# Kernel tuning notes

Hardware: AMD Instinct MI355X
Metric: run time of the kernel (lower is better)

## Reference

```python
import jax, jax.numpy as jnp
import numpy as np
from jax import lax

SCALES = [0.5, 1, 2]


def resize_bilinear_ac(x, oh, ow):
    """F.interpolate(mode='bilinear', align_corners=True) for NCHW x."""
    B, C, H, W = x.shape
    def coords(n_in, n_out):
        c = jnp.linspace(0.0, n_in - 1.0, n_out).astype(x.dtype)
        i0 = jnp.clip(jnp.floor(c).astype(jnp.int32), 0, n_in - 1)
        i1 = jnp.minimum(i0 + 1, n_in - 1)
        return i0, i1, c - i0.astype(x.dtype)
    y0, y1, wy = coords(H, oh)
    x0, x1, wx = coords(W, ow)
    top = x[:, :, y0, :] * (1 - wy)[:, None] + x[:, :, y1, :] * wy[:, None]
    return top[:, :, :, x0] * (1 - wx) + top[:, :, :, x1] * wx


def interpolate4d(t, oh, ow):
    """Geometry.interpolate4d: bilinear resize of both spatial pairs of [b,h1,w1,h2,w2]."""
    b, h1, w1, h2, w2 = t.shape
    t = t.reshape(b, h1, w1, h2 * w2).transpose(0, 3, 1, 2)
    t = resize_bilinear_ac(t, oh, ow)            # [b, h2*w2, oh, ow]
    t = t.reshape(b, h2, w2, oh * ow).transpose(0, 3, 1, 2)
    t = resize_bilinear_ac(t, oh, ow)            # [b, oh*ow, oh, ow]
    return t.reshape(b, oh, ow, oh, ow)


def conv2d_same(x, w):
    return lax.conv_general_dilated(x, w, (1, 1), [(1, 1), (1, 1)],
                                    dimension_numbers=('NCHW', 'OIHW', 'NCHW'))


def conv3d_same(x, w, p):
    return lax.conv_general_dilated(x, w, (1, 1, 1), [(p, p)] * 3,
                                    dimension_numbers=('NCDHW', 'OIDHW', 'NCDHW'))


def fast4d(corr, kernel, bias=None):
    """4D conv (stride 1, same zero-padding) via per-slice 3D convs, mirroring chm.fast4d.
    corr: [b, ci, sh, sw, th, tw]; kernel: [co, ci, k, k, k, k]."""
    b, ci, sh, sw, th, tw = corr.shape
    co, k = kernel.shape[0], kernel.shape[2]
    p = k // 2
    x = corr.transpose(0, 2, 1, 3, 4, 5).reshape(b * sh, ci, sw, th, tw)
    out = jnp.zeros((b, co, sh, sw, th, tw), corr.dtype)
    for pidx in range(k):
        ic = conv3d_same(x, kernel[:, :, pidx], p)
        ic = ic.reshape(b, sh, co, sw, th, tw).transpose(0, 2, 1, 3, 4, 5)
        a0, a1 = max(p - pidx, 0), min(sh, sh + p - pidx)
        s0, s1 = max(pidx - p, 0), min(sh, sh + pidx - p)
        out = out.at[:, :, a0:a1].add(ic[:, :, s0:s1])
    if bias is not None:
        out = out + bias.reshape(1, co, 1, 1, 1, 1)
    return out


def chm6d(corr, kernel):
    """6D conv with kernel (K,K,kk,kk,kk,kk), same zero-padding, no bias (chm.fast6d).
    corr: [b, 1, S, S, h, w, h, w]; kernel: [1, 1, K, K, kk, kk, kk, kk]."""
    b, _, S, _, h, w, _, _ = corr.shape
    K, kk = kernel.shape[2], kernel.shape[4]
    pk = K // 2
    x = corr.transpose(0, 2, 3, 1, 4, 5, 6, 7).reshape(b * S * S, 1, h, w, h, w)
    ker = kernel.reshape(1, K * K, kk, kk, kk, kk).swapaxes(0, 1)  # [K*K, 1, kk...]
    y = fast4d(x, ker).reshape(b, S, S, K * K, h, w, h, w)
    yp = jnp.pad(y, ((0, 0), (pk, pk), (pk, pk), (0, 0), (0, 0), (0, 0), (0, 0), (0, 0)))
    out = jnp.zeros((b, S, S, h, w, h, w), corr.dtype)
    for ki in range(K):
        for kj in range(K):
            out = out + yp[:, ki:ki + S, kj:kj + S, ki * K + kj]
    return out[:, None]


def mutual_nn_filter(cm):
    smax = jnp.max(cm, axis=2, keepdims=True)
    tmax = jnp.max(cm, axis=1, keepdims=True)
    smax = jnp.where(smax == 0, 1e-30, smax)
    tmax = jnp.where(tmax == 0, 1e-30, tmax)
    return cm * ((cm / smax) * (cm / tmax))


def build_correlation6d(src_feat, trg_feat, conv_ws):
    bsz, _, side, _ = src_feat.shape
    sfs, tfs = [], []
    for scale, w in zip(SCALES, conv_ws):
        s = int(np.floor(scale * side))
        sfs.append(conv2d_same(resize_bilinear_ac(src_feat, s, s), w))
        tfs.append(conv2d_same(resize_bilinear_ac(trg_feat, s, s), w))
    corr6d = []
    for sf in sfs:
        ch, ss = sf.shape[1], sf.shape[-1]
        sv = sf.reshape(bsz, ch, ss * ss).transpose(0, 2, 1)   # [b, ss^2, ch]
        sn = jnp.linalg.norm(sv, axis=2, keepdims=True)
        for tf in tfs:
            ts = tf.shape[-1]
            tv = tf.reshape(bsz, ch, ts * ts)                  # [b, ch, ts^2]
            tn = jnp.linalg.norm(tv, axis=1, keepdims=True)
            c = jnp.einsum('bsc,bct->bst', sv, tv) / (sn * tn)
            corr6d.append(interpolate4d(c.reshape(bsz, ss, ss, ts, ts), side, side))
    corr = jnp.stack(corr6d).reshape(3, 3, bsz, side, side, side, side)
    corr = corr.transpose(2, 0, 1, 3, 4, 5, 6)                 # [b, 3, 3, s, s, s, s]
    return jnp.maximum(corr, 0.0)


def chm_forward(src_feat, trg_feat, w0, w1, w2, k6, k4, b4):
    bsz, _, side, _ = src_feat.shape
    corr = build_correlation6d(src_feat, trg_feat, (w0, w1, w2))[:, None]
    corr = jax.nn.sigmoid(chm6d(corr, k6))                     # [b,1,3,3,h,w,h,w]
    h = w = side
    corr = corr.reshape(bsz, -1, h, w, h, w).max(axis=1)       # max over 9 scale pairs
    corr = interpolate4d(corr, 2 * h, 2 * w)[:, None]          # [b,1,2h,2w,2h,2w]
    corr = jax.nn.softplus(fast4d(corr, k4, b4)[:, 0])
    n = corr.shape[-1] ** 2
    return mutual_nn_filter(corr.reshape(bsz, n, n))


def setup_inputs() -> dict:
    key = jax.random.key(0)
    ks = jax.random.split(key, 8)
    b, fd, side = 4, 1024, 16
    w_std = 0.02  # ~kaiming for 3x3 conv with fan_in 1024*9
    return {
        'src_feat': jax.random.normal(ks[0], (b, fd, side, side), jnp.float32),
        'trg_feat': jax.random.normal(ks[1], (b, fd, side, side), jnp.float32),
        'conv_w0': jax.random.normal(ks[2], (fd // 4, fd, 3, 3), jnp.float32) * w_std,
        'conv_w1': jax.random.normal(ks[3], (fd // 4, fd, 3, 3), jnp.float32) * w_std,
        'conv_w2': jax.random.normal(ks[4], (fd // 4, fd, 3, 3), jnp.float32) * w_std,
        'chm6d_w': jax.random.normal(ks[5], (1, 1, 3, 3, 5, 5, 5, 5), jnp.float32) * 0.05,
        'chm4d_w': jax.random.normal(ks[6], (1, 1, 5, 5, 5, 5), jnp.float32) * 0.05,
        'chm4d_b': jnp.zeros((1,), jnp.float32),
    }


def reference(src_feat, trg_feat, conv_w0, conv_w1, conv_w2, chm6d_w, chm4d_w, chm4d_b):
    return chm_forward(src_feat, trg_feat, conv_w0, conv_w1, conv_w2, chm6d_w, chm4d_w, chm4d_b)
```

## Files before the change

### kernel.cpp

```cpp
#include <hip/hip_runtime.h>
#include <cstdint>
#include <cstddef>


#define DEVFN __device__ __forceinline__

typedef __attribute__((ext_vector_type(8))) short short8v;
typedef __attribute__((ext_vector_type(4))) float f32x4;
typedef unsigned int u32;

DEVFN void gl_lds16(const void* g, void* l){
  __builtin_amdgcn_global_load_lds(
      (const __attribute__((address_space(1))) u32*)g,
      (__attribute__((address_space(3))) u32*)l, 16, 0, 0);
}

constexpr size_t OFF_WB    = 0;
constexpr size_t OFF_P8    = 3538944;
constexpr size_t OFF_P16   = 3948544;
constexpr size_t OFF_P32   = 5275648;
constexpr size_t OFF_SF8   = 10010624;
constexpr size_t OFF_TF8   = 10076160;
constexpr size_t OFF_SF16  = 10141696;
constexpr size_t OFF_TF16  = 10403840;
constexpr size_t OFF_SF32  = 10665984;
constexpr size_t OFF_TF32  = 11714560;
constexpr size_t OFF_INVS  = 12763136;
constexpr size_t OFF_INVT  = 12768512;
constexpr size_t OFF_SMAX  = 12773888;
constexpr size_t OFF_TMAX  = 12777984;
constexpr size_t OFF_CORR6 = 12782080;
constexpr size_t OFF_CMAXP = OFF_CORR6 + 2359296 + 128;
constexpr size_t OFF_WA    = OFF_CMAXP + 131072;
constexpr size_t OFF_PARTK = OFF_WA + 96128;
constexpr size_t WS_FLOATS = OFF_PARTK + 2752512;

__device__ constexpr size_t PAIR_OFF[9] = {
  OFF_WB + 0,       OFF_WB + 16384,   OFF_WB + 81920,
  OFF_WB + 344064,  OFF_WB + 409600,  OFF_WB + 671744,
  OFF_WB + 1720320, OFF_WB + 1982464, OFF_WB + 3031040 };
constexpr size_t OFF_CL    = 0;
constexpr size_t OFF_MAXED = 9437184;
constexpr size_t OFF_INT32 = 262144;
constexpr size_t OFF_FB    = OFF_PARTK;

__device__ constexpr int SSARR[3] = {8, 16, 32};
__device__ constexpr int PAIR_START[9] = {0,4,20,84,100,164,420,484,740};

DEVFN unsigned short f2bf(float f){
  unsigned int u = __float_as_uint(f);
  return (unsigned short)((u + 0x7fffu + ((u >> 16) & 1u)) >> 16);
}
DEVFN float bf2f(unsigned short u){
  return __uint_as_float(((unsigned int)u) << 16);
}

__global__ __launch_bounds__(256) void k_wpack(const float* __restrict__ w0,
                                               const float* __restrict__ w1,
                                               const float* __restrict__ w2,
                                               float* __restrict__ wsf){
  int bx = blockIdx.x;
  int scale = bx >> 8, cg = (bx >> 4) & 15, ig = bx & 15;
  const float* w = (scale==0) ? w0 : (scale==1 ? w1 : w2);
  const int t = threadIdx.x;
  __shared__ float sW[16*580];
  const float* src = w + (size_t)cg*16*9216 + (size_t)ig*576;
  for (int i=t; i<9216; i+=256){
    int co = i/576, r = i%576;
    sW[co*580 + r] = src[(size_t)co*9216 + r];
  }
  __syncthreads();
  unsigned short* ob = (unsigned short*)(wsf + OFF_WB) + (size_t)scale*2359296;
  for (int f=t; f<1152; f+=256){
    int tap = f/128, rem = f%128, kcl = rem>>6, l = rem&63;
    int kc = ig*2 + kcl;
    int co = l & 15;
    int ciL = kcl*32 + ((l>>4)&3)*8;
    unsigned short* o = ob + ((size_t)tap*32768 + (size_t)kc*1024 + (size_t)cg*64 + l)*8;
    #pragma unroll
    for (int i=0;i<8;i++)
      o[i] = f2bf(sW[co*580 + (ciL+i)*9 + tap]);
  }
}

__global__ void k_wa(const float* __restrict__ k6, float* __restrict__ wsf){
  int gid = blockIdx.x*256 + threadIdx.x;
  if (gid >= 24000) return;
  int tap = gid / 192, rem = gid % 192;
  int kc = rem / 64, l = rem % 64;
  int d = tap % 5, ac = tap / 5, a = ac / 5, c = ac % 5;
  int so = l & 15, k8 = (l >> 4) * 8;
  unsigned short* o = (unsigned short*)(wsf + OFF_WA) + (size_t)gid*8;
  #pragma unroll
  for (int i=0;i<8;i++){
    int kg = kc*32 + k8 + i;
    int e = kg >> 4, pr = kg & 15;
    float v = 0.f;
    if (so < 9 && pr < 9 && e < 5){
      int pi = pr/3, pj = pr%3, sio = so/3, sjo = so%3;
      int ki = pi - sio + 1, kj = pj - sjo + 1;
      if (ki>=0 && ki<=2 && kj>=0 && kj<=2)
        v = k6[(((((ki*3+kj)*5 + a)*5 + c)*5 + d)*5) + e];
    }
    o[i] = f2bf(v);
  }
}

__global__ __launch_bounds__(256) void k_inpack(const float* __restrict__ src,
                                                const float* __restrict__ trg,
                                                float* __restrict__ wsf){
  int bt = blockIdx.x >> 6, cg = blockIdx.x & 63;
  int chbase = cg*16;
  int t = threadIdx.x;
  __shared__ float sIn[16][257];
  const float* gin = ((bt>=4)? trg : src) + ((size_t)(bt&3)*1024 + chbase)*256;
  #pragma unroll
  for (int i=0;i<16;i++){
    int idx = t + i*256; int ch = idx>>8, pos = idx&255;
    sIn[ch][pos] = gin[(size_t)ch*256 + pos];
  }
  __syncthreads();
  int ch = t & 15, pw = t >> 4;
  #pragma unroll 1
  for (int s=0; s<3; s++){
    int S = SSARR[s], Sp = S+2, Sp2 = Sp*Sp;
    size_t poff = (s==0)?OFF_P8 : (s==1)?OFF_P16 : OFF_P32;
    unsigned short* o = (unsigned short*)(wsf + poff) + (size_t)bt*Sp2*1024 + chbase + ch;
    float rs = 15.f/(float)(S-1);
    for (int i = pw; i < Sp2; i += 16){
      int py = i / Sp, px = i % Sp;
      float v = 0.f;
      if (py>0 && py<Sp-1 && px>0 && px<Sp-1){
        float cy = (float)(py-1)*rs, cx = (float)(px-1)*rs;
        int y0 = (int)cy; if (y0>15) y0=15; int y1 = (y0+1<16)?y0+1:15; float fy = cy-(float)y0;
        int x0 = (int)cx; if (x0>15) x0=15; int x1 = (x0+1<16)?x0+1:15; float fx = cx-(float)x0;
        v = (1.f-fy)*((1.f-fx)*sIn[ch][y0*16+x0] + fx*sIn[ch][y0*16+x1])
          +       fy*((1.f-fx)*sIn[ch][y1*16+x0] + fx*sIn[ch][y1*16+x1]);
      }
      o[(size_t)i*1024] = f2bf(v);
    }
  }
}

__global__ __launch_bounds__(256) void k_conv_mfma(float* __restrict__ wsf){
  int bs = (blockIdx.x & 7)*84 + (blockIdx.x >> 3);
  const int ks = bs & 1;
  int bx = bs >> 1;
  int scale, bt, cot, post, S, lgS;
  if (bx < 256)      { scale=2; S=32; lgS=5; bt=bx>>5; cot=(bx>>4)&1; post=bx&15; }
  else if (bx < 320) { int r=bx-256; scale=1; S=16; lgS=4; bt=r>>3; cot=(r>>2)&1; post=r&3; }
  else               { int r=bx-320; scale=0; S=8;  lgS=3; bt=r>>1; cot=r&1; post=0; }
  const int Sp = S+2, N = S*S;
  const unsigned short* WbS = (const unsigned short*)(wsf + OFF_WB) + (size_t)scale*2359296;
  size_t poff = scale==0?OFF_P8: scale==1?OFF_P16:OFF_P32;
  const unsigned short* Pb = (const unsigned short*)(wsf + poff) + (size_t)bt*Sp*Sp*1024;
  size_t obase = (scale==2) ? (bt>=4?OFF_TF32:OFF_SF32)
               : (scale==1) ? (bt>=4?OFF_TF16:OFF_SF16)
                            : (bt>=4?OFF_TF8 :OFF_SF8);
  if (ks) obase += OFF_PARTK - OFF_SF8;
  float* outp = wsf + obase + (size_t)(bt&3)*256*N;

  const int t = threadIdx.x, l = t&63, w = t>>6, wm = w&1, wn = w>>1;
  const int nc_base = cot*8;
  const int pos0 = post*64;
  const int it0 = ks*72, it1 = it0 + 72;

  __shared__ __align__(16) unsigned short Ab[2][8192];
  __shared__ __align__(16) unsigned short Bb[2][4096];

  f32x4 acc[4][2];
  #pragma unroll
  for (int i=0;i<4;i++)
    #pragma unroll
    for (int j=0;j<2;j++) acc[i][j] = (f32x4){0.f,0.f,0.f,0.f};

  auto STAGE = [&](int buf, int it){
    int tap = it>>4, kq = it&15;
    int dy = tap/3, dx = tap - dy*3;
    #pragma unroll
    for (int j=0;j<4;++j){
      int c = w + j*4;
      int kc = c>>3, nc = c&7;
      const unsigned short* src =
        WbS + ((((size_t)tap*32 + kq*2 + kc)*16 + nc_base + nc)*64 + l)*8;
      gl_lds16(src, &Ab[buf][c*512]);
    }
    #pragma unroll
    for (int j=0;j<2;++j){
      int c = w + j*4;
      int kc = c>>2, np = c&3;
      int pos = pos0 + np*16 + (l&15);
      int y = pos>>lgS, x = pos&(S-1);
      int row = (y+dy)*Sp + (x+dx);
      int ci = kq*64 + kc*32 + ((l>>4)<<3);
      gl_lds16(Pb + (size_t)row*1024 + ci, &Bb[buf][c*512]);
    }
  };

  STAGE(0, it0);
  __syncthreads();
  int buf = 0;
  #pragma unroll 1
  for (int it=it0; it<it1; ++it){
    if (it+1 < it1) STAGE(buf^1, it+1);
    #pragma unroll
    for (int kc=0; kc<2; ++kc){
      short8v a0 = *(const short8v*)&Ab[buf][((kc*8 + wm*4 + 0)*64 + l)*8];
      short8v a1 = *(const short8v*)&Ab[buf][((kc*8 + wm*4 + 1)*64 + l)*8];
      short8v a2 = *(const short8v*)&Ab[buf][((kc*8 + wm*4 + 2)*64 + l)*8];
      short8v a3 = *(const short8v*)&Ab[buf][((kc*8 + wm*4 + 3)*64 + l)*8];
      short8v b0 = *(const short8v*)&Bb[buf][((kc*4 + wn*2 + 0)*64 + l)*8];
      short8v b1 = *(const short8v*)&Bb[buf][((kc*4 + wn*2 + 1)*64 + l)*8];
      acc[0][0] = __builtin_amdgcn_mfma_f32_16x16x32_bf16(a0, b0, acc[0][0], 0,0,0);
      acc[1][0] = __builtin_amdgcn_mfma_f32_16x16x32_bf16(a1, b0, acc[1][0], 0,0,0);
      acc[2][0] = __builtin_amdgcn_mfma_f32_16x16x32_bf16(a2, b0, acc[2][0], 0,0,0);
      acc[3][0] = __builtin_amdgcn_mfma_f32_16x16x32_bf16(a3, b0, acc[3][0], 0,0,0);
      acc[0][1] = __builtin_amdgcn_mfma_f32_16x16x32_bf16(a0, b1, acc[0][1], 0,0,0);
      acc[1][1] = __builtin_amdgcn_mfma_f32_16x16x32_bf16(a1, b1, acc[1][1], 0,0,0);
      acc[2][1] = __builtin_amdgcn_mfma_f32_16x16x32_bf16(a2, b1, acc[2][1], 0,0,0);
      acc[3][1] = __builtin_amdgcn_mfma_f32_16x16x32_bf16(a3, b1, acc[3][1], 0,0,0);
    }
    __syncthreads();
    buf ^= 1;
  }

  const int r0 = (l>>4)*4, cl = l&15;
  float* ob = outp + (size_t)(cot*128 + wm*64)*N + pos0 + wn*32 + cl;
  #pragma unroll
  for (int mf=0; mf<4; ++mf)
    #pragma unroll
    for (int nf=0; nf<2; ++nf){
      float* op = ob + (size_t)(mf*16 + r0)*N + nf*16;
      #pragma unroll
      for (int i=0;i<4;++i) op[(size_t)i*N] = acc[mf][nf][i];
    }
}

__global__ void k_combine(float* __restrict__ ws){
  int i = blockIdx.x*256 + threadIdx.x;
  ws[OFF_SF8 + i] += ws[OFF_PARTK + i];
}

__global__ __launch_bounds__(256) void k_fbpack(float* __restrict__ ws){
  int bx = blockIdx.x;
  int tsr = bx/84, r = bx%84;
  int s, b, chunk;
  if (r < 4)       { s=0; b=r;        chunk=0; }
  else if (r < 20) { s=1; int q=r-4;  b=q>>2; chunk=q&3; }
  else             { s=2; int q=r-20; b=q>>4; chunk=q&15; }
  int P = SSARR[s]*SSARR[s];
  size_t fbase = (s==0)? (tsr?OFF_TF8 :OFF_SF8)
               : (s==1)? (tsr?OFF_TF16:OFF_SF16)
                       : (tsr?OFF_TF32:OFF_SF32);
  const float* src = ws + fbase + (size_t)b*256*P;
  int pos0 = chunk*64;
  const int t = threadIdx.x;
  __shared__ float tile[64][260];
  for (int i=0;i<64;i++){
    int idx = t + i*256; int ch = idx>>6, pl = idx&63;
    tile[pl][ch] = src[(size_t)ch*P + pos0 + pl];
  }
  __syncthreads();
  int rowbase = tsr*5376 + (s==0?0: s==1?256:1280) + b*P + pos0;
  unsigned short* FB = (unsigned short*)(ws + OFF_FB);
  for (int i=0;i<64;i++){
    int idx = t + i*256; int pl = idx>>8, ch = idx&255;
    FB[(size_t)(rowbase+pl)*256 + ch] = f2bf(tile[pl][ch]);
  }
}

__global__ void k_invnorm(float* __restrict__ ws){
  int gid = blockIdx.x*256 + threadIdx.x;
  int row = gid >> 4, sub = gid & 15;
  const unsigned short* fb = (const unsigned short*)(ws + OFF_FB)
                           + (size_t)row*256 + sub*16;
  float s = 0.f;
  #pragma unroll
  for (int i=0;i<2;i++){
    short8v v = *(const short8v*)(fb + i*8);
    #pragma unroll
    for (int j=0;j<8;j++){
      float f = bf2f(((unsigned short*)&v)[j]);
      s = fmaf(f, f, s);
    }
  }
  #pragma unroll
  for (int m=1; m<16; m<<=1) s += __shfl_xor(s, m);
  if (sub == 0){
    int tsr = row/5376, r = row%5376;
    ws[(tsr ? OFF_INVT : OFF_INVS) + r] = 1.f/sqrtf(s);
  }
}

__global__ __launch_bounds__(256) void k_corr(float* __restrict__ ws){
  int bx = blockIdx.x;
  int p = (bx>=4)+(bx>=20)+(bx>=84)+(bx>=100)+(bx>=164)+(bx>=420)+(bx>=484)+(bx>=740);
  int si = p/3, ti = p%3;
  int M = SSARR[si]*SSARR[si], N = SSARR[ti]*SSARR[ti];
  int ntN = N >> 6;
  int rem = bx - PAIR_START[p];
  int b = rem & 3; rem >>= 2;
  int nt = rem % ntN, mt = rem / ntN;
  int m0 = mt*64, n0 = nt*64;
  const unsigned short* FB = (const unsigned short*)(ws + OFF_FB);
  const unsigned short* Ap = FB + (size_t)((si==0?0: si==1?256:1280) + b*M + m0)*256;
  const unsigned short* Bp = FB + (size_t)(5376 + (ti==0?0: ti==1?256:1280) + b*N + n0)*256;
  const int t = threadIdx.x, l = t&63, w = t>>6, wm = w&1, wn = w>>1;
  const int mrow = wm*32 + (l&15), ncol = wn*32 + (l&15);
  f32x4 acc[2][2];
  #pragma unroll
  for (int i=0;i<2;i++)
    #pragma unroll
    for (int j=0;j<2;j++) acc[i][j] = (f32x4){0.f,0.f,0.f,0.f};
  #pragma unroll
  for (int ksp=0; ksp<8; ++ksp){
    const int ko = ksp*32 + ((l>>4)&3)*8;
    short8v a0 = *(const short8v*)(Ap + (size_t) mrow     *256 + ko);
    short8v a1 = *(const short8v*)(Ap + (size_t)(mrow+16) *256 + ko);
    short8v b0 = *(const short8v*)(Bp + (size_t) ncol     *256 + ko);
    short8v b1 = *(const short8v*)(Bp + (size_t)(ncol+16) *256 + ko);
    acc[0][0] = __builtin_amdgcn_mfma_f32_16x16x32_bf16(a0, b0, acc[0][0], 0,0,0);
    acc[1][0] = __builtin_amdgcn_mfma_f32_16x16x32_bf16(a1, b0, acc[1][0], 0,0,0);
    acc[0][1] = __builtin_amdgcn_mfma_f32_16x16x32_bf16(a0, b1, acc[0][1], 0,0,0);
    acc[1][1] = __builtin_amdgcn_mfma_f32_16x16x32_bf16(a1, b1, acc[1][1], 0,0,0);
  }
  const float* iS = ws + OFF_INVS + (si==0?0: si==1?256:1280) + (size_t)b*M;
  const float* iT = ws + OFF_INVT + (ti==0?0: ti==1?256:1280) + (size_t)b*N;
  float* C = ws + PAIR_OFF[p] + (size_t)b*M*N;
  const int r0 = (l>>4)*4, cl = l&15;
  #pragma unroll
  for (int mf=0; mf<2; ++mf)
    #pragma unroll
    for (int nf=0; nf<2; ++nf)
      #pragma unroll
      for (int i=0;i<4;++i){
        int m = m0 + wm*32 + mf*16 + r0 + i;
        int n = n0 + wn*32 + nf*16 + cl;
        C[(size_t)m*N + n] = acc[mf][nf][i]*iS[m]*iT[n];
      }
}

DEVFN void cw_coord(int i, int n, int OH, int& i0, int& i1, float& f){
  float c = (float)(i*(n-1))/(float)(OH-1);
  int a = (int)c; if (a > n-1) a = n-1;
  i0 = a; i1 = (a+1 < n) ? a+1 : n-1; f = c - (float)a;
}

__global__ __launch_bounds__(256) void k_interp_pairs(float* __restrict__ ws){
  int bx = blockIdx.x;
  int p = bx >> 10;
  int bl = bx & 1023;
  int b = bl >> 8, oy = (bl >> 4) & 15, ox = bl & 15;
  int si = p/3, ti = p%3;
  int h1 = SSARR[si], t1 = SSARR[ti], t12 = t1*t1;
  int y0,y1,x0,x1; float fy,fx;
  cw_coord(oy,h1,16,y0,y1,fy); cw_coord(ox,h1,16,x0,x1,fx);
  const float* in = ws + PAIR_OFF[p] + (size_t)b*h1*h1*t12;
  __shared__ float sPl[4][1024];
  const int t = threadIdx.x;
  {
    const float* pl0 = in + (size_t)(y0*h1+x0)*t12;
    const float* pl1 = in + (size_t)(y0*h1+x1)*t12;
    const float* pl2 = in + (size_t)(y1*h1+x0)*t12;
    const float* pl3 = in + (size_t)(y1*h1+x1)*t12;
    for (int i=t; i<t12; i+=256){
      sPl[0][i] = pl0[i]; sPl[1][i] = pl1[i];
      sPl[2][i] = pl2[i]; sPl[3][i] = pl3[i];
    }
  }
  __syncthreads();
  int px = t & 15, py = t >> 4;
  int u0,u1,v0,v1; float fu,fv;
  cw_coord(py,t1,16,u0,u1,fu); cw_coord(px,t1,16,v0,v1,fv);
  float wY[2]={1.f-fy,fy}, wX[2]={1.f-fx,fx};
  float wU[2]={1.f-fu,fu}, wV[2]={1.f-fv,fv};
  int us[2]={u0,u1}, vs[2]={v0,v1};
  float s = 0.f;
  #pragma unroll
  for (int qa=0; qa<2; qa++)
    #pragma unroll
    for (int qc=0; qc<2; qc++){
      float wyx = wY[qa]*wX[qc];
      const float* base = sPl[qa*2+qc];
      #pragma unroll
      for (int qu=0; qu<2; qu++)
        #pragma unroll
        for (int qv=0; qv<2; qv++)
          s += wyx*wU[qu]*wV[qv]*base[us[qu]*t1 + vs[qv]];
    }
  ws[OFF_CORR6 + ((size_t)b*9 + p)*65536 + ((size_t)(oy*16+ox)<<8) + t] = fmaxf(s, 0.f);
}

__global__ __launch_bounds__(256) void k_cl(float* __restrict__ ws){
  int bx = blockIdx.x;
  int b = bx >> 8, yx = bx & 255;
  const int t = threadIdx.x;
  __shared__ __align__(16) unsigned short tile[10080];
  for (int i=t; i<1260; i+=256)
    *reinterpret_cast<f32x4*>((float*)&tile[i*8]) = (f32x4){0.f,0.f,0.f,0.f};
  __syncthreads();
  const float* c6 = ws + OFF_CORR6 + ((size_t)b*9 << 16) + ((size_t)yx << 8);
  const int qy = t >> 4, qx = t & 15;
  const int wo = ((2+qy)*21 + 2+qx)*24;
  #pragma unroll
  for (int pr=0; pr<9; ++pr)
    tile[wo + pr] = f2bf(c6[((size_t)pr << 16) + t]);
  __syncthreads();
  unsigned short* o = (unsigned short*)(ws + OFF_CL) + (size_t)bx*10080;
  for (int i=t; i<1260; i+=256)
    *reinterpret_cast<f32x4*>((float*)&o[i*8]) =
      *reinterpret_cast<const f32x4*>((const float*)&tile[i*8]);
}

__global__ __launch_bounds__(256) void k_chm6d(float* __restrict__ ws){
  int id = (blockIdx.x & 7)*128 + (blockIdx.x >> 3);
  const int b = id >> 8, sy = (id >> 4) & 15, sx = id & 15;
  const int t = threadIdx.x, l = t & 63, w = t >> 6;
  const int x = l & 15, h = (l >> 4) & 1, e2 = (l >> 4) >> 1;
  const unsigned short* CLu = (const unsigned short*)(ws + OFF_CL);
  const unsigned short* WAu = (const unsigned short*)(ws + OFF_WA);
  __shared__ __align__(16) unsigned short tile[2][10080];

  f32x4 acc[4];
  #pragma unroll
  for (int i=0;i<4;i++) acc[i] = (f32x4){0.f,0.f,0.f,0.f};

  auto STAGE = [&](int buf, int YX){
    const unsigned short* src = CLu + (size_t)(b*256 + YX)*10080;
    #pragma unroll
    for (int j=0;j<5;++j){
      int ch = t + j*256;
      if (ch < 1260) gl_lds16(src + (size_t)ch*8, &tile[buf][ch*8]);
    }
  };

  const int xb0 = (x + e2)*24 + 8*h;

  int i0 = 0;
  for (; i0 < 25; ++i0){
    int Y = sy + i0/5 - 2, X = sx + i0%5 - 2;
    if (Y>=0 && Y<=15 && X>=0 && X<=15) break;
  }
  {
    int Y = sy + i0/5 - 2, X = sx + i0%5 - 2;
    STAGE(0, Y*16 + X);
  }
  __syncthreads();
  int buf = 0, i = i0;
  #pragma unroll 1
  while (i < 25){
    int nx = i + 1;
    for (; nx < 25; ++nx){
      int Y = sy + nx/5 - 2, X = sx + nx%5 - 2;
      if (Y>=0 && Y<=15 && X>=0 && X<=15) break;
    }
    if (nx < 25){
      int Y = sy + nx/5 - 2, X = sx + nx%5 - 2;
      STAGE(buf^1, Y*16 + X);
    }
    {
      const unsigned short* wa = WAu + (size_t)i*5*3*512;
      short8v afr[5][3];
      #pragma unroll
      for (int d=0; d<5; ++d)
        #pragma unroll
        for (int kc=0; kc<3; ++kc)
          afr[d][kc] = *(const short8v*)&wa[((d*3 + kc)*64 + l)*8];
      const unsigned short* tb = &tile[buf][0];
      #pragma unroll
      for (int rl=0; rl<8; ++rl){
        const int row = (w*4 + rl)*504;
        short8v bf0 = *(const short8v*)&tb[row + xb0];
        short8v bf1 = *(const short8v*)&tb[row + xb0 + 48];
        short8v bf2 = *(const short8v*)&tb[row + xb0 + 96];
        #pragma unroll
        for (int y=0; y<4; ++y){
          if (y <= rl && rl - y <= 4){
            const int d = rl - y;
            acc[y] = __builtin_amdgcn_mfma_f32_16x16x32_bf16(afr[d][0], bf0, acc[y], 0,0,0);
            acc[y] = __builtin_amdgcn_mfma_f32_16x16x32_bf16(afr[d][1], bf1, acc[y], 0,0,0);
            acc[y] = __builtin_amdgcn_mfma_f32_16x16x32_bf16(afr[d][2], bf2, acc[y], 0,0,0);
          }
        }
      }
    }
    __syncthreads();
    buf ^= 1; i = nx;
  }

  const int g = l >> 4;
  float* maxed = ws + OFF_MAXED + (size_t)b*65536 + (size_t)(sy*16+sx)*256;
  #pragma unroll
  for (int y=0; y<4; ++y){
    float lm;
    if (g < 2)      lm = fmaxf(fmaxf(acc[y][0], acc[y][1]), fmaxf(acc[y][2], acc[y][3]));
    else if (g==2)  lm = acc[y][0];
    else            lm = -1e30f;
    lm = fmaxf(lm, __shfl_xor(lm, 16));
    lm = fmaxf(lm, __shfl_xor(lm, 32));
    if (l < 16)
      maxed[(w*4 + y)*16 + x] = 1.f/(1.f + expf(-lm));
  }
}

__global__ void k_interp32(float* __restrict__ ws){
  int id = blockIdx.x*256 + threadIdx.x;
  int px = id & 31, py = (id>>5)&31, ox = (id>>10)&31, oy = (id>>15)&31, b = id>>20;
  int y0,y1,x0,x1,u0,u1,v0,v1; float fy,fx,fu,fv;
  cw_coord(oy,16,32,y0,y1,fy); cw_coord(ox,16,32,x0,x1,fx);
  cw_coord(py,16,32,u0,u1,fu); cw_coord(px,16,32,v0,v1,fv);
  const float* in = ws + OFF_MAXED + (size_t)b*65536;
  int ys[2]={y0,y1}, xs[2]={x0,x1}, us[2]={u0,u1}, vs[2]={v0,v1};
  float wy[2]={1.f-fy,fy}, wx[2]={1.f-fx,fx}, wu[2]={1.f-fu,fu}, wv[2]={1.f-fv,fv};
  float s = 0.f;
  #pragma unroll
  for (int ia=0; ia<2; ia++)
    #pragma unroll
    for (int ic=0; ic<2; ic++){
      float wyx = wy[ia]*wx[ic];
      const float* base = in + ((size_t)ys[ia]*16 + xs[ic])*256;
      #pragma unroll
      for (int id_=0; id_<2; id_++)
        #pragma unroll
        for (int ie=0; ie<2; ie++)
          s += wyx*wu[id_]*wv[ie]*base[(size_t)us[id_]*16 + vs[ie]];
    }
  ws[OFF_INT32 + id] = s;
}

__global__ __launch_bounds__(256) void k_fast4d(float* __restrict__ ws,
                                                const float* __restrict__ k4,
                                                const float* __restrict__ b4,
                                                float* __restrict__ out){
  const int b = blockIdx.y;
  const int sy = blockIdx.x >> 3, sx0 = (blockIdx.x & 7) << 2;
  const int t = threadIdx.x;
  const int y = t >> 3, x0 = (t & 7) << 2;
  __shared__ __align__(16) float sQ[2][36*48];
  __shared__ float red[256];
  for (int i=t; i<1728; i+=256){ sQ[0][i]=0.f; sQ[1][i]=0.f; }
  __syncthreads();
  const float* in = ws + OFF_INT32 + (size_t)b*1048576;
  float acc[4][4] = {};

  int i0 = 0;
  for (; i0 < 40; ++i0){
    int Y = sy + (i0>>3) - 2, X = sx0 - 2 + (i0&7);
    if (Y>=0 && Y<=31 && X>=0 && X<=31) break;
  }
  float4 pf = make_float4(0.f,0.f,0.f,0.f);
  if (i0 < 40){
    int Y = sy + (i0>>3) - 2, X = sx0 - 2 + (i0&7);
    pf = *reinterpret_cast<const float4*>(in + (size_t)(Y*32+X)*1024 + t*4);
  }
  int cur = 0, i = i0;
  const int srow = t >> 3, scol4 = (t & 7) << 2;
  const int wo = (2+srow)*48 + 4 + scol4;
  #pragma unroll 1
  while (i < 40){
    int nx = i+1;
    for (; nx < 40; ++nx){
      int Y = sy + (nx>>3) - 2, X = sx0 - 2 + (nx&7);
      if (Y>=0 && Y<=31 && X>=0 && X<=31) break;
    }
    *reinterpret_cast<f32x4*>(&sQ[cur][wo]) = (f32x4){pf.x,pf.y,pf.z,pf.w};
    if (nx < 40){
      int Y = sy + (nx>>3) - 2, X = sx0 - 2 + (nx&7);
      pf = *reinterpret_cast<const float4*>(in + (size_t)(Y*32+X)*1024 + t*4);
    }
    __syncthreads();
    const int a = i>>3, Xi = i&7;
    const float* ka = k4 + a*125;
    #pragma unroll
    for (int d=0; d<5; d++){
      const float* row = &sQ[cur][(y+d)*48 + x0];
      float4 q0 = *reinterpret_cast<const float4*>(row);
      float4 q1 = *reinterpret_cast<const float4*>(row+4);
      float4 q2 = *reinterpret_cast<const float4*>(row+8);
      float r12[12] = {q0.x,q0.y,q0.z,q0.w, q1.x,q1.y,q1.z,q1.w,
                       q2.x,q2.y,q2.z,q2.w};
      #pragma unroll
      for (int j=0; j<4; j++){
        const int c = Xi - j;
        if (c >= 0 && c <= 4){
          const float* kc = ka + c*25 + d*5;
          #pragma unroll
          for (int e=0; e<5; e++){
            float wv = kc[e];
            #pragma unroll
            for (int xi=0; xi<4; xi++)
              acc[j][xi] = fmaf(r12[xi+e+2], wv, acc[j][xi]);
          }
        }
      }
    }
    cur ^= 1; i = nx;
  }
  float bias = b4[0];
  float rmax[4];
  #pragma unroll
  for (int j=0; j<4; j++){
    float4 o;
    float* po = &o.x;
    #pragma unroll
    for (int xi=0; xi<4; xi++){
      float xv = acc[j][xi] + bias;
      po[xi] = fmaxf(xv,0.f) + log1pf(expf(-fabsf(xv)));
    }
    rmax[j] = fmaxf(fmaxf(o.x,o.y), fmaxf(o.z,o.w));
    *reinterpret_cast<float4*>(
      out + ((size_t)b*1024 + sy*32 + sx0 + j)*1024 + y*32 + x0) = o;
  }
  #pragma unroll 1
  for (int j=0; j<4; j++){
    __syncthreads();
    red[t] = rmax[j];
    __syncthreads();
    for (int off=128; off; off>>=1){
      if (t < off) red[t] = fmaxf(red[t], red[t+off]);
      __syncthreads();
    }
    if (!t) ws[OFF_SMAX + (size_t)b*1024 + sy*32 + sx0 + j] = red[0];
  }
}

__global__ void k_colmax_p(const float* __restrict__ cm, float* __restrict__ ws){
  int b = blockIdx.x >> 7, rg = (blockIdx.x >> 2) & 31, cg = blockIdx.x & 3;
  int c = cg*256 + threadIdx.x;
  const float* base = cm + (size_t)b*1048576 + (size_t)rg*32768 + c;
  float m = -1e30f;
  #pragma unroll 4
  for (int r=0; r<32; r++) m = fmaxf(m, base[(size_t)r*1024]);
  ws[OFF_CMAXP + (size_t)(b*32+rg)*1024 + c] = m;
}

__global__ void k_colmax_r(float* __restrict__ ws){
  int id = blockIdx.x*256 + threadIdx.x;
  int b = id >> 10, c = id & 1023;
  float m = -1e30f;
  #pragma unroll
  for (int rg=0; rg<32; rg++)
    m = fmaxf(m, ws[OFF_CMAXP + (size_t)(b*32+rg)*1024 + c]);
  ws[OFF_TMAX + id] = m;
}

__global__ void k_mutual(float* __restrict__ cm, const float* __restrict__ ws){
  int id = blockIdx.x*256 + threadIdx.x;
  int b = id >> 20, r = (id>>10)&1023, c = id&1023;
  float v  = cm[id];
  float sm = ws[OFF_SMAX + (b<<10) + r];
  float tm = ws[OFF_TMAX + (b<<10) + c];
  sm = (sm==0.f) ? 1e-30f : sm;
  tm = (tm==0.f) ? 1e-30f : tm;
  cm[id] = v * (v/sm) * (v/tm);
}

extern "C" void kernel_launch(void* const* d_in, const int* in_sizes, int n_in,
                              void* d_out, int out_size, void* d_ws, size_t ws_size,
                              hipStream_t stream){
  const float* src = (const float*)d_in[0];
  const float* trg = (const float*)d_in[1];
  const float* w0  = (const float*)d_in[2];
  const float* w1  = (const float*)d_in[3];
  const float* w2  = (const float*)d_in[4];
  const float* k6  = (const float*)d_in[5];
  const float* k4  = (const float*)d_in[6];
  const float* b4  = (const float*)d_in[7];
  float* ws  = (float*)d_ws;
  float* out = (float*)d_out;
  (void)in_sizes; (void)n_in; (void)out_size; (void)ws_size;

  k_wpack       <<<768,   256, 0, stream>>>(w0, w1, w2, ws);
  k_wa          <<<94,    256, 0, stream>>>(k6, ws);
  k_inpack      <<<512,   256, 0, stream>>>(src, trg, ws);
  k_conv_mfma   <<<672,   256, 0, stream>>>(ws);
  k_combine     <<<10752, 256, 0, stream>>>(ws);
  k_fbpack      <<<168,   256, 0, stream>>>(ws);
  k_invnorm     <<<672,   256, 0, stream>>>(ws);
  k_corr        <<<1764,  256, 0, stream>>>(ws);
  k_interp_pairs<<<9216,  256, 0, stream>>>(ws);
  k_cl          <<<1024,  256, 0, stream>>>(ws);
  k_chm6d       <<<1024,  256, 0, stream>>>(ws);
  k_interp32    <<<16384, 256, 0, stream>>>(ws);
  k_fast4d      <<<dim3(256,4),  256, 0, stream>>>(ws, k4, b4, out);
  k_colmax_p    <<<512,   256, 0, stream>>>(out, ws);
  k_colmax_r    <<<16,    256, 0, stream>>>(ws);
  k_mutual      <<<16384, 256, 0, stream>>>(out, ws);
}
```

Measured before the change: 415.5 us.

## Recast the final 4D convolution as bf16 MFMA with prepacked banded weights

The scalar-FMA 4D conv (5^4 taps over a 32^4 volume) becomes a bf16 MFMA kernel. A new pre-kernel packs the 4D kernel into a banded A-matrix covering the a and c offsets for a 4x4 tile of source positions. Each block stages a bf16 tile of the interpolated volume in LDS once instead of streaming it through a double-buffered loop. The row max now comes from wave shuffles into per-block partials, which k_mutual combines. This trades fp32 accuracy for bf16 inputs, and the padded band adds redundant MACs.

Measured after the change: 377.1 us. 9.3% less time.

```diff
diff --git a/kernel.cpp b/kernel.cpp
--- a/kernel.cpp
+++ b/kernel.cpp
@@ -27,13 +27,14 @@
 constexpr size_t OFF_TF32  = 11714560;
 constexpr size_t OFF_INVS  = 12763136;
 constexpr size_t OFF_INVT  = 12768512;
-constexpr size_t OFF_SMAX  = 12773888;
 constexpr size_t OFF_TMAX  = 12777984;
 constexpr size_t OFF_CORR6 = 12782080;
 constexpr size_t OFF_CMAXP = OFF_CORR6 + 2359296 + 128;
 constexpr size_t OFF_WA    = OFF_CMAXP + 131072;
 constexpr size_t OFF_PARTK = OFF_WA + 96128;
-constexpr size_t WS_FLOATS = OFF_PARTK + 2752512;
+constexpr size_t OFF_SMAXP = OFF_PARTK + 2752512;
+constexpr size_t OFF_WA4   = OFF_SMAXP + 16384;
+constexpr size_t WS_FLOATS = OFF_WA4 + 12800;
 
 __device__ constexpr size_t PAIR_OFF[9] = {
   OFF_WB + 0,       OFF_WB + 16384,   OFF_WB + 81920,
@@ -102,6 +103,25 @@
       if (ki>=0 && ki<=2 && kj>=0 && kj<=2)
         v = k6[(((((ki*3+kj)*5 + a)*5 + c)*5 + d)*5) + e];
     }
+    o[i] = f2bf(v);
+  }
+}
+
+__global__ void k_wa4(const float* __restrict__ k4, float* __restrict__ wsf){
+  int gid = blockIdx.x*256 + threadIdx.x;
+  if (gid >= 3200) return;
+  int d = gid / 640, rem = gid % 640;
+  int kc = rem / 64, l = rem % 64;
+  int so = l & 15, soy = so >> 2, sox = so & 3;
+  int e = kc >> 1;
+  int pyw = 4*(kc & 1) + (l >> 4);
+  unsigned short* o = (unsigned short*)(wsf + OFF_WA4) + (size_t)gid*8;
+  #pragma unroll
+  for (int i=0;i<8;i++){
+    int a = pyw - soy, c = i - sox;
+    float v = 0.f;
+    if (a>=0 && a<=4 && c>=0 && c<=4)
+      v = k4[((a*5 + c)*5 + d)*5 + e];
     o[i] = f2bf(v);
   }
 }
@@ -529,98 +549,90 @@
 }
 
 __global__ __launch_bounds__(256) void k_fast4d(float* __restrict__ ws,
-                                                const float* __restrict__ k4,
                                                 const float* __restrict__ b4,
                                                 float* __restrict__ out){
-  const int b = blockIdx.y;
-  const int sy = blockIdx.x >> 3, sx0 = (blockIdx.x & 7) << 2;
-  const int t = threadIdx.x;
-  const int y = t >> 3, x0 = (t & 7) << 2;
-  __shared__ __align__(16) float sQ[2][36*48];
-  __shared__ float red[256];
-  for (int i=t; i<1728; i+=256){ sQ[0][i]=0.f; sQ[1][i]=0.f; }
-  __syncthreads();
-  const float* in = ws + OFF_INT32 + (size_t)b*1048576;
-  float acc[4][4] = {};
-
-  int i0 = 0;
-  for (; i0 < 40; ++i0){
-    int Y = sy + (i0>>3) - 2, X = sx0 - 2 + (i0&7);
-    if (Y>=0 && Y<=31 && X>=0 && X<=31) break;
-  }
-  float4 pf = make_float4(0.f,0.f,0.f,0.f);
-  if (i0 < 40){
-    int Y = sy + (i0>>3) - 2, X = sx0 - 2 + (i0&7);
-    pf = *reinterpret_cast<const float4*>(in + (size_t)(Y*32+X)*1024 + t*4);
-  }
-  int cur = 0, i = i0;
-  const int srow = t >> 3, scol4 = (t & 7) << 2;
-  const int wo = (2+srow)*48 + 4 + scol4;
+  int id = (blockIdx.x & 7)*128 + (blockIdx.x >> 3);
+  const int b = id >> 8, rem = id & 255;
+  const int syb = rem >> 5, sxb = (rem >> 2) & 7, yh = rem & 3;
+  const int t = threadIdx.x, l = t & 63, w = t >> 6;
+  __shared__ __align__(16) unsigned short T[27648];
+  __shared__ float red[4][16];
+  for (int i=t; i<3456; i+=256)
+    *reinterpret_cast<f32x4*>((float*)&T[i*8]) = (f32x4){0.f,0.f,0.f,0.f};
+  __syncthreads();
+  const float* I = ws + OFF_INT32 + (size_t)b*1048576;
+  #pragma unroll 4
+  for (int j=0; j<48; ++j){
+    int idx2 = j*256 + t;
+    int xo = idx2 & 15, pl = (idx2>>4) & 63, ry = idx2 >> 10;
+    int pya = syb*4 + (pl>>3) - 2;
+    int pxa = sxb*4 + (pl&7) - 2;
+    int rya = yh*8 + ry - 2;
+    if (pya>=0 && pya<32 && pxa>=0 && pxa<32 && rya>=0 && rya<32){
+      float2 v = *reinterpret_cast<const float2*>(
+          I + (size_t)(pya*32+pxa)*1024 + rya*32 + xo*2);
+      int base = (ry*36 + xo*2 + 2)*64 + pl;
+      T[base]      = f2bf(v.x);
+      T[base + 64] = f2bf(v.y);
+    }
+  }
+  __syncthreads();
+  const unsigned short* WA4 = (const unsigned short*)(ws + OFF_WA4);
+  f32x4 acc[2][2];
+  #pragma unroll
+  for (int i=0;i<2;i++)
+    #pragma unroll
+    for (int j=0;j<2;j++) acc[i][j] = (f32x4){0.f,0.f,0.f,0.f};
+  const unsigned short* Tl = T + (l&15)*64 + (l>>4)*8 + w*2*2304;
   #pragma unroll 1
-  while (i < 40){
-    int nx = i+1;
-    for (; nx < 40; ++nx){
-      int Y = sy + (nx>>3) - 2, X = sx0 - 2 + (nx&7);
-      if (Y>=0 && Y<=31 && X>=0 && X<=31) break;
-    }
-    *reinterpret_cast<f32x4*>(&sQ[cur][wo]) = (f32x4){pf.x,pf.y,pf.z,pf.w};
-    if (nx < 40){
-      int Y = sy + (nx>>3) - 2, X = sx0 - 2 + (nx&7);
-      pf = *reinterpret_cast<const float4*>(in + (size_t)(Y*32+X)*1024 + t*4);
-    }
-    __syncthreads();
-    const int a = i>>3, Xi = i&7;
-    const float* ka = k4 + a*125;
-    #pragma unroll
-    for (int d=0; d<5; d++){
-      const float* row = &sQ[cur][(y+d)*48 + x0];
-      float4 q0 = *reinterpret_cast<const float4*>(row);
-      float4 q1 = *reinterpret_cast<const float4*>(row+4);
-      float4 q2 = *reinterpret_cast<const float4*>(row+8);
-      float r12[12] = {q0.x,q0.y,q0.z,q0.w, q1.x,q1.y,q1.z,q1.w,
-                       q2.x,q2.y,q2.z,q2.w};
+  for (int d=0; d<5; ++d){
+    short8v afr[10];
+    #pragma unroll
+    for (int kc=0; kc<10; ++kc)
+      afr[kc] = *(const short8v*)&WA4[((size_t)(d*10 + kc)*64 + l)*8];
+    #pragma unroll
+    for (int y2=0; y2<2; ++y2){
+      const unsigned short* Tr = Tl + (y2 + d)*2304;
       #pragma unroll
-      for (int j=0; j<4; j++){
-        const int c = Xi - j;
-        if (c >= 0 && c <= 4){
-          const float* kc = ka + c*25 + d*5;
-          #pragma unroll
-          for (int e=0; e<5; e++){
-            float wv = kc[e];
-            #pragma unroll
-            for (int xi=0; xi<4; xi++)
-              acc[j][xi] = fmaf(r12[xi+e+2], wv, acc[j][xi]);
-          }
+      for (int xg=0; xg<2; ++xg){
+        const unsigned short* Tx = Tr + xg*1024;
+        #pragma unroll
+        for (int kc=0; kc<10; ++kc){
+          short8v bf = *(const short8v*)&Tx[(kc>>1)*64 + (kc&1)*32];
+          acc[y2][xg] = __builtin_amdgcn_mfma_f32_16x16x32_bf16(afr[kc], bf, acc[y2][xg], 0,0,0);
         }
       }
     }
-    cur ^= 1; i = nx;
-  }
-  float bias = b4[0];
-  float rmax[4];
-  #pragma unroll
-  for (int j=0; j<4; j++){
-    float4 o;
-    float* po = &o.x;
-    #pragma unroll
-    for (int xi=0; xi<4; xi++){
-      float xv = acc[j][xi] + bias;
-      po[xi] = fmaxf(xv,0.f) + log1pf(expf(-fabsf(xv)));
-    }
-    rmax[j] = fmaxf(fmaxf(o.x,o.y), fmaxf(o.z,o.w));
-    *reinterpret_cast<float4*>(
-      out + ((size_t)b*1024 + sy*32 + sx0 + j)*1024 + y*32 + x0) = o;
-  }
-  #pragma unroll 1
-  for (int j=0; j<4; j++){
-    __syncthreads();
-    red[t] = rmax[j];
-    __syncthreads();
-    for (int off=128; off; off>>=1){
-      if (t < off) red[t] = fmaxf(red[t], red[t+off]);
-      __syncthreads();
-    }
-    if (!t) ws[OFF_SMAX + (size_t)b*1024 + sy*32 + sx0 + j] = red[0];
+  }
+  const float bias = b4[0];
+  float rm[4] = {-1e30f,-1e30f,-1e30f,-1e30f};
+  #pragma unroll
+  for (int y2=0; y2<2; ++y2)
+    #pragma unroll
+    for (int xg=0; xg<2; ++xg)
+      #pragma unroll
+      for (int i=0; i<4; ++i){
+        int so = (l>>4)*4 + i;
+        float xv = acc[y2][xg][i] + bias;
+        float sp = fmaxf(xv,0.f) + log1pf(expf(-fabsf(xv)));
+        int row = (syb*4 + (so>>2))*32 + sxb*4 + (so&3);
+        int col = (yh*8 + w*2 + y2)*32 + xg*16 + (l&15);
+        out[((size_t)b*1024 + row)*1024 + col] = sp;
+        rm[i] = fmaxf(rm[i], sp);
+      }
+  #pragma unroll
+  for (int m=1; m<16; m<<=1)
+    #pragma unroll
+    for (int i=0;i<4;++i) rm[i] = fmaxf(rm[i], __shfl_xor(rm[i], m));
+  if ((l & 15) == 0){
+    #pragma unroll
+    for (int i=0;i<4;++i) red[w][(l>>4)*4 + i] = rm[i];
+  }
+  __syncthreads();
+  if (t < 16){
+    float m = fmaxf(fmaxf(red[0][t], red[1][t]), fmaxf(red[2][t], red[3][t]));
+    int row = (syb*4 + (t>>2))*32 + sxb*4 + (t&3);
+    ws[OFF_SMAXP + (size_t)yh*4096 + (size_t)b*1024 + row] = m;
   }
 }
 
@@ -648,7 +660,9 @@
   int id = blockIdx.x*256 + threadIdx.x;
   int b = id >> 20, r = (id>>10)&1023, c = id&1023;
   float v  = cm[id];
-  float sm = ws[OFF_SMAX + (b<<10) + r];
+  size_t si = (size_t)(b<<10) + r;
+  float sm = fmaxf(fmaxf(ws[OFF_SMAXP + si],        ws[OFF_SMAXP + 4096 + si]),
+                   fmaxf(ws[OFF_SMAXP + 8192 + si], ws[OFF_SMAXP + 12288 + si]));
   float tm = ws[OFF_TMAX + (b<<10) + c];
   sm = (sm==0.f) ? 1e-30f : sm;
   tm = (tm==0.f) ? 1e-30f : tm;
@@ -672,6 +686,7 @@
 
   k_wpack       <<<768,   256, 0, stream>>>(w0, w1, w2, ws);
   k_wa          <<<94,    256, 0, stream>>>(k6, ws);
+  k_wa4         <<<13,    256, 0, stream>>>(k4, ws);
   k_inpack      <<<512,   256, 0, stream>>>(src, trg, ws);
   k_conv_mfma   <<<672,   256, 0, stream>>>(ws);
   k_combine     <<<10752, 256, 0, stream>>>(ws);
@@ -682,7 +697,7 @@
   k_cl          <<<1024,  256, 0, stream>>>(ws);
   k_chm6d       <<<1024,  256, 0, stream>>>(ws);
   k_interp32    <<<16384, 256, 0, stream>>>(ws);
-  k_fast4d      <<<dim3(256,4),  256, 0, stream>>>(ws, k4, b4, out);
+  k_fast4d      <<<1024,  256, 0, stream>>>(ws, b4, out);
   k_colmax_p    <<<512,   256, 0, stream>>>(out, ws);
   k_colmax_r    <<<16,    256, 0, stream>>>(ws);
   k_mutual      <<<16384, 256, 0, stream>>>(out, ws);
```
